# Kernel optimization log

Measured on AMD Instinct MI355X. Metric: run time of the kernel, lower is better.

The kernel has to match this reference:

```python
import jax, jax.numpy as jnp
import numpy as np

B, H, L, DK = 1, 16, 2048, 64
F_FACTOR = 64            # f
MAX_SEQ = 2048           # max_seq_len
RB = MAX_SEQ // F_FACTOR # 32, out dim of f_b


def setup_inputs() -> dict:
    key = jax.random.key(0)
    ks = jax.random.split(key, 6)
    q = jax.random.normal(ks[0], (B, H, L, DK), dtype=jnp.float32)
    v = jax.random.normal(ks[1], (B, H, L, DK), dtype=jnp.float32)
    # nn.Linear weights: [out_features, in_features]
    Wa = jax.random.normal(ks[2], (F_FACTOR, DK), dtype=jnp.float32) / np.sqrt(DK)
    ba = jax.random.normal(ks[3], (F_FACTOR,), dtype=jnp.float32) * 0.02
    Wb = jax.random.normal(ks[4], (RB, DK), dtype=jnp.float32) / np.sqrt(DK)
    bb = jax.random.normal(ks[5], (RB,), dtype=jnp.float32) * 0.02
    return {"q": q, "v": v, "Wa": Wa, "ba": ba, "Wb": Wb, "bb": bb, "len_q": L}


def reference(q, v, Wa, ba, Wb, bb, len_q):
    f = Wa.shape[0]            # f
    rb = Wb.shape[0]           # max_seq_len // f
    # h_a: repeat each of the f factor channels (max_seq_len//f) times -> [B,H,L,max_seq_len], slice to len_q
    h_a = jnp.repeat(q @ Wa.T + ba, rb, axis=-1)[..., :len_q]
    # h_b: repeat each of the (max_seq_len//f) channels f times
    h_b = jnp.repeat(q @ Wb.T + bb, f, axis=-1)[..., :len_q]
    # dense_attn = h_a @ h_b^T  -> [B,H,L,L]
    dense_attn = jnp.einsum('bhik,bhjk->bhij', h_a, h_b)
    # mask=None path; dropout inactive (eval / p=0)
    dense_attn = jax.nn.softmax(dense_attn, axis=-1)
    output = jnp.matmul(dense_attn, v)  # [B,H,L,DK]
    return (output, dense_attn)
```

## Files before the change

kernel.cpp:

```cpp
#include <hip/hip_runtime.h>
#include <hip/hip_bf16.h>


#define HN 16
#define LN 2048
#define KR 32

typedef __attribute__((ext_vector_type(8))) short bf16x8;
typedef __attribute__((ext_vector_type(4))) float f32x4;

__device__ __forceinline__ float b2f(unsigned short u) {
    return __uint_as_float(((unsigned int)u) << 16);
}
__device__ __forceinline__ unsigned short f2b(float f) {
    __hip_bfloat16 h = __float2bfloat16(f);
    return *reinterpret_cast<unsigned short*>(&h);
}

__device__ __forceinline__ void bar_lds() {
    __builtin_amdgcn_sched_barrier(0);
    asm volatile("s_waitcnt lgkmcnt(0)" ::: "memory");
    __builtin_amdgcn_s_barrier();
    __builtin_amdgcn_sched_barrier(0);
}

#define TILE_B 4096
#define TILE_V 4096

__global__ __launch_bounds__(256) void k_cb(
    const float* __restrict__ q,
    const float* __restrict__ Wa, const float* __restrict__ ba,
    const float* __restrict__ Wb, const float* __restrict__ bb,
    unsigned short* __restrict__ Chi, unsigned short* __restrict__ Clo,
    unsigned short* __restrict__ TileB)
{
    __shared__ float sWa[64 * 64];
    __shared__ float sWb[32 * 64];
    __shared__ float sba[64];
    __shared__ float sbb[32];
    const int tid = threadIdx.x;
    for (int i = tid; i < 64 * 64; i += 256) sWa[i] = Wa[i];
    for (int i = tid; i < 32 * 64; i += 256) sWb[i] = Wb[i];
    if (tid < 64) sba[tid] = ba[tid];
    if (tid < 32) sbb[tid] = bb[tid];
    __syncthreads();

    const int t = blockIdx.x * 256 + tid;
    const int row = t >> 2, kg = t & 3, mh = kg * 8;
    const int h = row >> 11, i = row & 2047;
    const int jc = i >> 6, c = i & 63;

    float qf[64];
    const float4* q4p = reinterpret_cast<const float4*>(q + (size_t)row * 64);
    #pragma unroll
    for (int k4 = 0; k4 < 16; ++k4) {
        float4 u = q4p[k4];
        qf[4*k4+0] = u.x; qf[4*k4+1] = u.y; qf[4*k4+2] = u.z; qf[4*k4+3] = u.w;
    }
    unsigned short chb[8], clb[8], bhb[8], blb[8];
    #pragma unroll
    for (int mi = 0; mi < 8; ++mi) {
        const int m = mh + mi;
        float a0 = sba[2*m], a1 = sba[2*m+1], bv = sbb[m];
        const float4* wa0 = reinterpret_cast<const float4*>(&sWa[(2*m) * 64]);
        const float4* wa1 = reinterpret_cast<const float4*>(&sWa[(2*m+1) * 64]);
        const float4* wb0 = reinterpret_cast<const float4*>(&sWb[m * 64]);
        #pragma unroll
        for (int k4 = 0; k4 < 16; ++k4) {
            float4 w0 = wa0[k4], w1 = wa1[k4], w2 = wb0[k4];
            float x0 = qf[4*k4], x1 = qf[4*k4+1], x2 = qf[4*k4+2], x3 = qf[4*k4+3];
            a0 = fmaf(x0, w0.x, a0); a0 = fmaf(x1, w0.y, a0);
            a0 = fmaf(x2, w0.z, a0); a0 = fmaf(x3, w0.w, a0);
            a1 = fmaf(x0, w1.x, a1); a1 = fmaf(x1, w1.y, a1);
            a1 = fmaf(x2, w1.z, a1); a1 = fmaf(x3, w1.w, a1);
            bv = fmaf(x0, w2.x, bv); bv = fmaf(x1, w2.y, bv);
            bv = fmaf(x2, w2.z, bv); bv = fmaf(x3, w2.w, bv);
        }
        float cc = 32.f * (a0 + a1);
        unsigned short ch = f2b(cc);
        chb[mi] = ch; clb[mi] = f2b(cc - b2f(ch));
        unsigned short bh = f2b(bv);
        bhb[mi] = bh; blb[mi] = f2b(bv - b2f(bh));
    }
    *reinterpret_cast<uint4*>(Chi + (size_t)row * KR + mh) = *reinterpret_cast<uint4*>(chb);
    *reinterpret_cast<uint4*>(Clo + (size_t)row * KR + mh) = *reinterpret_cast<uint4*>(clb);
    unsigned short* tb = TileB + (size_t)(h * 32 + jc) * TILE_B + (kg * 64 + c) * 8;
    *reinterpret_cast<uint4*>(tb)        = *reinterpret_cast<uint4*>(bhb);
    *reinterpret_cast<uint4*>(tb + 2048) = *reinterpret_cast<uint4*>(blb);
}

__global__ __launch_bounds__(256) void k_vtc(
    const float* __restrict__ v, unsigned short* __restrict__ TileV)
{
    __shared__ unsigned short sv[64 * 66];
    const int tid = threadIdx.x;
    const int h = blockIdx.x >> 5, jc = blockIdx.x & 31;
    const float* src = v + (size_t)(h * LN + jc * 64) * 64;
    for (int i = tid; i < 4096; i += 256)
        sv[(i >> 6) * 66 + (i & 63)] = f2b(src[i]);
    __syncthreads();
    unsigned short* vt = TileV + (size_t)(h * 32 + jc) * TILE_V;
    #pragma unroll
    for (int it = 0; it < 2; ++it) {
        const int gi = tid + it * 256;
        const int jg = gi >> 6, d = gi & 63;
        unsigned short g8[8];
        #pragma unroll
        for (int jj = 0; jj < 8; ++jj)
            g8[jj] = sv[(jg * 8 + jj) * 66 + d];
        *reinterpret_cast<uint4*>(vt + (jg * 64 + d) * 8) = *reinterpret_cast<uint4*>(g8);
    }
}

#define PS_STRIDE 1032
__global__ __launch_bounds__(256, 2) void k_fuse(
    const unsigned short* __restrict__ Chi, const unsigned short* __restrict__ Clo,
    const unsigned short* __restrict__ TileB, const unsigned short* __restrict__ TileV,
    float* __restrict__ outO, float* __restrict__ outP)
{
    __shared__ unsigned short ps[16 * PS_STRIDE];
    __shared__ float sRedM[4][16];
    __shared__ float sRedL[4][16];

    const int b = blockIdx.x;
    const int h = (b & 7) * 2 + (b >> 10);
    const int tile = (b >> 3) & 127;
    const int tid = threadIdx.x, w = tid >> 6, lane = tid & 63;
    const int quad = lane >> 4, n16 = lane & 15;
    const int rbase = tile * 16;
    const int hL = h * LN;

    const bf16x8 ahi = *reinterpret_cast<const bf16x8*>(Chi + (size_t)(hL + rbase + n16) * KR + quad * 8);
    const bf16x8 alo = *reinterpret_cast<const bf16x8*>(Clo + (size_t)(hL + rbase + n16) * KR + quad * 8);

    const unsigned short* bTile = TileB + (size_t)(h * 32) * TILE_B;
    const unsigned short* vTile = TileV + (size_t)(h * 32) * TILE_V;
    const int fragW = (quad * 64 + w * 16 + n16) * 8;

    f32x4 zero = {0.f, 0.f, 0.f, 0.f};
    f32x4 sS[32];

    #pragma unroll
    for (int jc = 0; jc < 32; ++jc) {
        const unsigned short* g = bTile + jc * TILE_B;
        bf16x8 bhi = *reinterpret_cast<const bf16x8*>(g + fragW);
        bf16x8 blo = *reinterpret_cast<const bf16x8*>(g + 2048 + fragW);
        f32x4 acc = zero;
        acc = __builtin_amdgcn_mfma_f32_16x16x32_bf16(ahi, bhi, acc, 0, 0, 0);
        acc = __builtin_amdgcn_mfma_f32_16x16x32_bf16(ahi, blo, acc, 0, 0, 0);
        acc = __builtin_amdgcn_mfma_f32_16x16x32_bf16(alo, bhi, acc, 0, 0, 0);
        sS[jc] = acc;
    }

    float mr[4], li[4], liS;
    const int srow = w * 4 + quad;
    {
        float m0[4];
        #pragma unroll
        for (int r = 0; r < 4; ++r) {
            float mm = sS[0][r];
            #pragma unroll
            for (int jc = 1; jc < 32; ++jc) mm = fmaxf(mm, sS[jc][r]);
            #pragma unroll
            for (int off = 1; off <= 8; off <<= 1)
                mm = fmaxf(mm, __shfl_xor(mm, off, 64));
            m0[r] = mm;
        }
        if (n16 == 0) {
            #pragma unroll
            for (int r = 0; r < 4; ++r) sRedM[w][quad * 4 + r] = m0[r];
        }
        bar_lds();
        #pragma unroll
        for (int r = 0; r < 4; ++r)
            mr[r] = fmaxf(fmaxf(sRedM[0][quad*4+r], sRedM[1][quad*4+r]),
                          fmaxf(sRedM[2][quad*4+r], sRedM[3][quad*4+r]));
        float l0[4] = {0.f, 0.f, 0.f, 0.f};
        #pragma unroll
        for (int jc = 0; jc < 32; ++jc) {
            #pragma unroll
            for (int r = 0; r < 4; ++r) {
                float p = __expf(sS[jc][r] - mr[r]);
                sS[jc][r] = p;
                l0[r] += p;
            }
        }
        #pragma unroll
        for (int r = 0; r < 4; ++r) {
            float ll = l0[r];
            #pragma unroll
            for (int off = 1; off <= 8; off <<= 1)
                ll += __shfl_xor(ll, off, 64);
            l0[r] = ll;
        }
        if (n16 == 0) {
            #pragma unroll
            for (int r = 0; r < 4; ++r) sRedL[w][quad * 4 + r] = l0[r];
        }
        bar_lds();
        #pragma unroll
        for (int r = 0; r < 4; ++r)
            li[r] = 1.f / (sRedL[0][quad*4+r] + sRedL[1][quad*4+r]
                         + sRedL[2][quad*4+r] + sRedL[3][quad*4+r]);
        liS = 1.f / (sRedL[0][srow] + sRedL[1][srow]
                   + sRedL[2][srow] + sRedL[3][srow]);
    }

    f32x4 o0 = zero, o1 = zero;
    float* prow = outP + (size_t)(hL + rbase + srow) * LN;
    #pragma unroll
    for (int half = 0; half < 2; ++half) {
        if (half) bar_lds();
        const int jc0 = half * 16;
        #pragma unroll
        for (int ji = 0; ji < 16; ++ji) {
            #pragma unroll
            for (int r = 0; r < 4; ++r)
                ps[(quad * 4 + r) * PS_STRIDE + ji * 64 + w * 16 + n16]
                    = f2b(sS[jc0 + ji][r]);
        }
        bar_lds();

        #pragma unroll
        for (int ji = 0; ji < 16; ++ji) {
            const int jc = jc0 + ji;
            const unsigned short* vt = vTile + jc * TILE_V;
            bf16x8 pa0 = *reinterpret_cast<const bf16x8*>(
                ps + n16 * PS_STRIDE + ji * 64 + quad * 8);
            bf16x8 pa1 = *reinterpret_cast<const bf16x8*>(
                ps + n16 * PS_STRIDE + ji * 64 + 32 + quad * 8);
            bf16x8 vb0 = *reinterpret_cast<const bf16x8*>(
                vt + (quad * 64 + w * 16 + n16) * 8);
            bf16x8 vb1 = *reinterpret_cast<const bf16x8*>(
                vt + ((4 + quad) * 64 + w * 16 + n16) * 8);
            o0 = __builtin_amdgcn_mfma_f32_16x16x32_bf16(pa0, vb0, o0, 0, 0, 0);
            o1 = __builtin_amdgcn_mfma_f32_16x16x32_bf16(pa1, vb1, o1, 0, 0, 0);
        }

        #pragma unroll
        for (int ch = 0; ch < 16; ++ch) {
            const unsigned short* pp = ps + srow * PS_STRIDE + ch * 64 + n16 * 4;
            uint2 u = *reinterpret_cast<const uint2*>(pp);
            f32x4 pv;
            pv[0] = __uint_as_float((u.x & 0xffffu) << 16) * liS;
            pv[1] = __uint_as_float(u.x & 0xffff0000u) * liS;
            pv[2] = __uint_as_float((u.y & 0xffffu) << 16) * liS;
            pv[3] = __uint_as_float(u.y & 0xffff0000u) * liS;
            __builtin_nontemporal_store(pv, reinterpret_cast<f32x4*>(
                prow + half * 1024 + ch * 64 + n16 * 4));
        }
    }
    #pragma unroll
    for (int r = 0; r < 4; ++r)
        __builtin_nontemporal_store((o0[r] + o1[r]) * li[r],
            &outO[(size_t)(hL + rbase + quad * 4 + r) * 64 + w * 16 + n16]);
}

extern "C" void kernel_launch(void* const* d_in, const int* in_sizes, int n_in,
                              void* d_out, int out_size, void* d_ws, size_t ws_size,
                              hipStream_t stream)
{
    (void)in_sizes; (void)n_in; (void)out_size; (void)ws_size;
    const float* q  = (const float*)d_in[0];
    const float* v  = (const float*)d_in[1];
    const float* Wa = (const float*)d_in[2];
    const float* ba = (const float*)d_in[3];
    const float* Wb = (const float*)d_in[4];
    const float* bb = (const float*)d_in[5];

    float* out = (float*)d_out;
    char* wsb = (char*)d_ws;
    const size_t MB = 1024 * 1024;
    unsigned short* Chi   = (unsigned short*)(wsb);
    unsigned short* Clo   = (unsigned short*)(wsb + 2 * MB);
    unsigned short* TileB = (unsigned short*)(wsb + 4 * MB);
    unsigned short* TileV = (unsigned short*)(wsb + 8 * MB);

    float* outO = out;
    float* outP = out + (size_t)HN * LN * 64;

    hipLaunchKernelGGL(k_cb, dim3(512), dim3(256), 0, stream,
                       q, Wa, ba, Wb, bb, Chi, Clo, TileB);
    hipLaunchKernelGGL(k_vtc, dim3(512), dim3(256), 0, stream, v, TileV);
    hipLaunchKernelGGL(k_fuse, dim3(2048), dim3(256), 0, stream,
                       Chi, Clo, TileB, TileV, outO, outP);
}
```

Before: 370.5 us.

## Merge prep kernels, pack softmax probs to bf16 registers, raise occupancy

```diff
diff --git a/kernel.cpp b/kernel.cpp
--- a/kernel.cpp
+++ b/kernel.cpp
@@ -27,18 +27,41 @@
 #define TILE_B 4096
 #define TILE_V 4096
 
-__global__ __launch_bounds__(256) void k_cb(
-    const float* __restrict__ q,
+__global__ __launch_bounds__(256) void k_prep(
+    const float* __restrict__ q, const float* __restrict__ v,
     const float* __restrict__ Wa, const float* __restrict__ ba,
     const float* __restrict__ Wb, const float* __restrict__ bb,
     unsigned short* __restrict__ Chi, unsigned short* __restrict__ Clo,
-    unsigned short* __restrict__ TileB)
+    unsigned short* __restrict__ TileB, unsigned short* __restrict__ TileV)
 {
     __shared__ float sWa[64 * 64];
     __shared__ float sWb[32 * 64];
     __shared__ float sba[64];
     __shared__ float sbb[32];
     const int tid = threadIdx.x;
+
+    if (blockIdx.x >= 512) {
+        unsigned short* sv = reinterpret_cast<unsigned short*>(sWa);
+        const int bb_ = blockIdx.x - 512;
+        const int h = bb_ >> 5, jc = bb_ & 31;
+        const float* src = v + (size_t)(h * LN + jc * 64) * 64;
+        for (int i = tid; i < 4096; i += 256)
+            sv[(i >> 6) * 66 + (i & 63)] = f2b(src[i]);
+        __syncthreads();
+        unsigned short* vt = TileV + (size_t)(h * 32 + jc) * TILE_V;
+        #pragma unroll
+        for (int it = 0; it < 2; ++it) {
+            const int gi = tid + it * 256;
+            const int jg = gi >> 6, d = gi & 63;
+            unsigned short g8[8];
+            #pragma unroll
+            for (int jj = 0; jj < 8; ++jj)
+                g8[jj] = sv[(jg * 8 + jj) * 66 + d];
+            *reinterpret_cast<uint4*>(vt + (jg * 64 + d) * 8) = *reinterpret_cast<uint4*>(g8);
+        }
+        return;
+    }
+
     for (int i = tid; i < 64 * 64; i += 256) sWa[i] = Wa[i];
     for (int i = tid; i < 32 * 64; i += 256) sWb[i] = Wb[i];
     if (tid < 64) sba[tid] = ba[tid];
@@ -89,31 +112,8 @@
     *reinterpret_cast<uint4*>(tb + 2048) = *reinterpret_cast<uint4*>(blb);
 }
 
-__global__ __launch_bounds__(256) void k_vtc(
-    const float* __restrict__ v, unsigned short* __restrict__ TileV)
-{
-    __shared__ unsigned short sv[64 * 66];
-    const int tid = threadIdx.x;
-    const int h = blockIdx.x >> 5, jc = blockIdx.x & 31;
-    const float* src = v + (size_t)(h * LN + jc * 64) * 64;
-    for (int i = tid; i < 4096; i += 256)
-        sv[(i >> 6) * 66 + (i & 63)] = f2b(src[i]);
-    __syncthreads();
-    unsigned short* vt = TileV + (size_t)(h * 32 + jc) * TILE_V;
-    #pragma unroll
-    for (int it = 0; it < 2; ++it) {
-        const int gi = tid + it * 256;
-        const int jg = gi >> 6, d = gi & 63;
-        unsigned short g8[8];
-        #pragma unroll
-        for (int jj = 0; jj < 8; ++jj)
-            g8[jj] = sv[(jg * 8 + jj) * 66 + d];
-        *reinterpret_cast<uint4*>(vt + (jg * 64 + d) * 8) = *reinterpret_cast<uint4*>(g8);
-    }
-}
-
 #define PS_STRIDE 1032
-__global__ __launch_bounds__(256, 2) void k_fuse(
+__global__ __launch_bounds__(256, 3) void k_fuse(
     const unsigned short* __restrict__ Chi, const unsigned short* __restrict__ Clo,
     const unsigned short* __restrict__ TileB, const unsigned short* __restrict__ TileV,
     float* __restrict__ outO, float* __restrict__ outP)
@@ -147,15 +147,16 @@
         bf16x8 blo = *reinterpret_cast<const bf16x8*>(g + 2048 + fragW);
         f32x4 acc = zero;
         acc = __builtin_amdgcn_mfma_f32_16x16x32_bf16(ahi, bhi, acc, 0, 0, 0);
+        acc = __builtin_amdgcn_mfma_f32_16x16x32_bf16(alo, bhi, acc, 0, 0, 0);
         acc = __builtin_amdgcn_mfma_f32_16x16x32_bf16(ahi, blo, acc, 0, 0, 0);
-        acc = __builtin_amdgcn_mfma_f32_16x16x32_bf16(alo, bhi, acc, 0, 0, 0);
         sS[jc] = acc;
     }
 
-    float mr[4], li[4], liS;
+    unsigned int pk[64];
+    float liS;
     const int srow = w * 4 + quad;
     {
-        float m0[4];
+        float m0[4], mr[4];
         #pragma unroll
         for (int r = 0; r < 4; ++r) {
             float mm = sS[0][r];
@@ -178,12 +179,13 @@
         float l0[4] = {0.f, 0.f, 0.f, 0.f};
         #pragma unroll
         for (int jc = 0; jc < 32; ++jc) {
-            #pragma unroll
-            for (int r = 0; r < 4; ++r) {
-                float p = __expf(sS[jc][r] - mr[r]);
-                sS[jc][r] = p;
-                l0[r] += p;
-            }
+            float p0 = __expf(sS[jc][0] - mr[0]);
+            float p1 = __expf(sS[jc][1] - mr[1]);
+            float p2 = __expf(sS[jc][2] - mr[2]);
+            float p3 = __expf(sS[jc][3] - mr[3]);
+            l0[0] += p0; l0[1] += p1; l0[2] += p2; l0[3] += p3;
+            pk[jc*2]   = ((unsigned int)f2b(p1) << 16) | (unsigned int)f2b(p0);
+            pk[jc*2+1] = ((unsigned int)f2b(p3) << 16) | (unsigned int)f2b(p2);
         }
         #pragma unroll
         for (int r = 0; r < 4; ++r) {
@@ -198,10 +200,6 @@
             for (int r = 0; r < 4; ++r) sRedL[w][quad * 4 + r] = l0[r];
         }
         bar_lds();
-        #pragma unroll
-        for (int r = 0; r < 4; ++r)
-            li[r] = 1.f / (sRedL[0][quad*4+r] + sRedL[1][quad*4+r]
-                         + sRedL[2][quad*4+r] + sRedL[3][quad*4+r]);
         liS = 1.f / (sRedL[0][srow] + sRedL[1][srow]
                    + sRedL[2][srow] + sRedL[3][srow]);
     }
@@ -214,12 +212,29 @@
         const int jc0 = half * 16;
         #pragma unroll
         for (int ji = 0; ji < 16; ++ji) {
-            #pragma unroll
-            for (int r = 0; r < 4; ++r)
-                ps[(quad * 4 + r) * PS_STRIDE + ji * 64 + w * 16 + n16]
-                    = f2b(sS[jc0 + ji][r]);
+            const int jc = jc0 + ji;
+            #pragma unroll
+            for (int r = 0; r < 4; ++r) {
+                const unsigned int pkv = pk[jc*2 + (r>>1)];
+                const unsigned short pv16 = (r & 1) ? (unsigned short)(pkv >> 16)
+                                                    : (unsigned short)(pkv & 0xffffu);
+                ps[(quad * 4 + r) * PS_STRIDE + ji * 64 + w * 16 + n16] = pv16;
+            }
         }
         bar_lds();
+
+        #pragma unroll
+        for (int ch = 0; ch < 16; ++ch) {
+            const unsigned short* pp = ps + srow * PS_STRIDE + ch * 64 + n16 * 4;
+            uint2 u = *reinterpret_cast<const uint2*>(pp);
+            f32x4 pv;
+            pv[0] = __uint_as_float((u.x & 0xffffu) << 16) * liS;
+            pv[1] = __uint_as_float(u.x & 0xffff0000u) * liS;
+            pv[2] = __uint_as_float((u.y & 0xffffu) << 16) * liS;
+            pv[3] = __uint_as_float(u.y & 0xffff0000u) * liS;
+            __builtin_nontemporal_store(pv, reinterpret_cast<f32x4*>(
+                prow + half * 1024 + ch * 64 + n16 * 4));
+        }
 
         #pragma unroll
         for (int ji = 0; ji < 16; ++ji) {
@@ -236,24 +251,14 @@
             o0 = __builtin_amdgcn_mfma_f32_16x16x32_bf16(pa0, vb0, o0, 0, 0, 0);
             o1 = __builtin_amdgcn_mfma_f32_16x16x32_bf16(pa1, vb1, o1, 0, 0, 0);
         }
-
-        #pragma unroll
-        for (int ch = 0; ch < 16; ++ch) {
-            const unsigned short* pp = ps + srow * PS_STRIDE + ch * 64 + n16 * 4;
-            uint2 u = *reinterpret_cast<const uint2*>(pp);
-            f32x4 pv;
-            pv[0] = __uint_as_float((u.x & 0xffffu) << 16) * liS;
-            pv[1] = __uint_as_float(u.x & 0xffff0000u) * liS;
-            pv[2] = __uint_as_float((u.y & 0xffffu) << 16) * liS;
-            pv[3] = __uint_as_float(u.y & 0xffff0000u) * liS;
-            __builtin_nontemporal_store(pv, reinterpret_cast<f32x4*>(
-                prow + half * 1024 + ch * 64 + n16 * 4));
-        }
-    }
-    #pragma unroll
-    for (int r = 0; r < 4; ++r)
-        __builtin_nontemporal_store((o0[r] + o1[r]) * li[r],
+    }
+    #pragma unroll
+    for (int r = 0; r < 4; ++r) {
+        const float li = 1.f / (sRedL[0][quad*4+r] + sRedL[1][quad*4+r]
+                              + sRedL[2][quad*4+r] + sRedL[3][quad*4+r]);
+        __builtin_nontemporal_store((o0[r] + o1[r]) * li,
             &outO[(size_t)(hL + rbase + quad * 4 + r) * 64 + w * 16 + n16]);
+    }
 }
 
 extern "C" void kernel_launch(void* const* d_in, const int* in_sizes, int n_in,
@@ -279,9 +284,8 @@
     float* outO = out;
     float* outP = out + (size_t)HN * LN * 64;
 
-    hipLaunchKernelGGL(k_cb, dim3(512), dim3(256), 0, stream,
-                       q, Wa, ba, Wb, bb, Chi, Clo, TileB);
-    hipLaunchKernelGGL(k_vtc, dim3(512), dim3(256), 0, stream, v, TileV);
+    hipLaunchKernelGGL(k_prep, dim3(1024), dim3(256), 0, stream,
+                       q, v, Wa, ba, Wb, bb, Chi, Clo, TileB, TileV);
     hipLaunchKernelGGL(k_fuse, dim3(2048), dim3(256), 0, stream,
                        Chi, Clo, TileB, TileV, outO, outP);
 }
```

Result: no change. 376.2 us (+1.5%).

## Split fused softmax-attention block into 8 waves across key halves

Applied to the files above, without the earlier changes.

```diff
diff --git a/kernel.cpp b/kernel.cpp
--- a/kernel.cpp
+++ b/kernel.cpp
@@ -112,21 +112,24 @@
     }
 }
 
-#define PS_STRIDE 1032
-__global__ __launch_bounds__(256, 2) void k_fuse(
+#define PS_STRIDE 2056
+__global__ __launch_bounds__(512, 4) void k_fuse(
     const unsigned short* __restrict__ Chi, const unsigned short* __restrict__ Clo,
     const unsigned short* __restrict__ TileB, const unsigned short* __restrict__ TileV,
     float* __restrict__ outO, float* __restrict__ outP)
 {
     __shared__ unsigned short ps[16 * PS_STRIDE];
-    __shared__ float sRedM[4][16];
-    __shared__ float sRedL[4][16];
+    __shared__ float sRedM[8][16];
+    __shared__ float sRedL[8][16];
+    __shared__ float sO[4 * 16 * 16];
 
     const int b = blockIdx.x;
     const int h = (b & 7) * 2 + (b >> 10);
     const int tile = (b >> 3) & 127;
     const int tid = threadIdx.x, w = tid >> 6, lane = tid & 63;
     const int quad = lane >> 4, n16 = lane & 15;
+    const int jh = w >> 2, sub = w & 3;
+    const int dg = w & 3;
     const int rbase = tile * 16;
     const int hL = h * LN;
 
@@ -135,32 +138,32 @@
 
     const unsigned short* bTile = TileB + (size_t)(h * 32) * TILE_B;
     const unsigned short* vTile = TileV + (size_t)(h * 32) * TILE_V;
-    const int fragW = (quad * 64 + w * 16 + n16) * 8;
+    const int fragW = (quad * 64 + sub * 16 + n16) * 8;
 
     f32x4 zero = {0.f, 0.f, 0.f, 0.f};
-    f32x4 sS[32];
-
-    #pragma unroll
-    for (int jc = 0; jc < 32; ++jc) {
-        const unsigned short* g = bTile + jc * TILE_B;
+    f32x4 sS[16];
+
+    #pragma unroll
+    for (int ji = 0; ji < 16; ++ji) {
+        const unsigned short* g = bTile + (jh * 16 + ji) * TILE_B;
         bf16x8 bhi = *reinterpret_cast<const bf16x8*>(g + fragW);
         bf16x8 blo = *reinterpret_cast<const bf16x8*>(g + 2048 + fragW);
         f32x4 acc = zero;
         acc = __builtin_amdgcn_mfma_f32_16x16x32_bf16(ahi, bhi, acc, 0, 0, 0);
+        acc = __builtin_amdgcn_mfma_f32_16x16x32_bf16(alo, bhi, acc, 0, 0, 0);
         acc = __builtin_amdgcn_mfma_f32_16x16x32_bf16(ahi, blo, acc, 0, 0, 0);
-        acc = __builtin_amdgcn_mfma_f32_16x16x32_bf16(alo, bhi, acc, 0, 0, 0);
-        sS[jc] = acc;
-    }
-
-    float mr[4], li[4], liS;
-    const int srow = w * 4 + quad;
+        sS[ji] = acc;
+    }
+
+    float li[4], liS;
+    const int srow = w * 2 + (lane >> 5);
     {
-        float m0[4];
+        float m0[4], mr[4];
         #pragma unroll
         for (int r = 0; r < 4; ++r) {
             float mm = sS[0][r];
             #pragma unroll
-            for (int jc = 1; jc < 32; ++jc) mm = fmaxf(mm, sS[jc][r]);
+            for (int ji = 1; ji < 16; ++ji) mm = fmaxf(mm, sS[ji][r]);
             #pragma unroll
             for (int off = 1; off <= 8; off <<= 1)
                 mm = fmaxf(mm, __shfl_xor(mm, off, 64));
@@ -172,16 +175,20 @@
         }
         bar_lds();
         #pragma unroll
-        for (int r = 0; r < 4; ++r)
-            mr[r] = fmaxf(fmaxf(sRedM[0][quad*4+r], sRedM[1][quad*4+r]),
-                          fmaxf(sRedM[2][quad*4+r], sRedM[3][quad*4+r]));
+        for (int r = 0; r < 4; ++r) {
+            float a = fmaxf(fmaxf(sRedM[0][quad*4+r], sRedM[1][quad*4+r]),
+                            fmaxf(sRedM[2][quad*4+r], sRedM[3][quad*4+r]));
+            float c = fmaxf(fmaxf(sRedM[4][quad*4+r], sRedM[5][quad*4+r]),
+                            fmaxf(sRedM[6][quad*4+r], sRedM[7][quad*4+r]));
+            mr[r] = fmaxf(a, c);
+        }
         float l0[4] = {0.f, 0.f, 0.f, 0.f};
         #pragma unroll
-        for (int jc = 0; jc < 32; ++jc) {
+        for (int ji = 0; ji < 16; ++ji) {
             #pragma unroll
             for (int r = 0; r < 4; ++r) {
-                float p = __expf(sS[jc][r] - mr[r]);
-                sS[jc][r] = p;
+                float p = __expf(sS[ji][r] - mr[r]);
+                sS[ji][r] = p;
                 l0[r] += p;
             }
         }
@@ -201,59 +208,71 @@
         #pragma unroll
         for (int r = 0; r < 4; ++r)
             li[r] = 1.f / (sRedL[0][quad*4+r] + sRedL[1][quad*4+r]
-                         + sRedL[2][quad*4+r] + sRedL[3][quad*4+r]);
-        liS = 1.f / (sRedL[0][srow] + sRedL[1][srow]
-                   + sRedL[2][srow] + sRedL[3][srow]);
-    }
-
-    f32x4 o0 = zero, o1 = zero;
-    float* prow = outP + (size_t)(hL + rbase + srow) * LN;
-    #pragma unroll
-    for (int half = 0; half < 2; ++half) {
-        if (half) bar_lds();
-        const int jc0 = half * 16;
-        #pragma unroll
-        for (int ji = 0; ji < 16; ++ji) {
-            #pragma unroll
-            for (int r = 0; r < 4; ++r)
-                ps[(quad * 4 + r) * PS_STRIDE + ji * 64 + w * 16 + n16]
-                    = f2b(sS[jc0 + ji][r]);
-        }
-        bar_lds();
-
-        #pragma unroll
-        for (int ji = 0; ji < 16; ++ji) {
-            const int jc = jc0 + ji;
-            const unsigned short* vt = vTile + jc * TILE_V;
-            bf16x8 pa0 = *reinterpret_cast<const bf16x8*>(
-                ps + n16 * PS_STRIDE + ji * 64 + quad * 8);
-            bf16x8 pa1 = *reinterpret_cast<const bf16x8*>(
-                ps + n16 * PS_STRIDE + ji * 64 + 32 + quad * 8);
-            bf16x8 vb0 = *reinterpret_cast<const bf16x8*>(
-                vt + (quad * 64 + w * 16 + n16) * 8);
-            bf16x8 vb1 = *reinterpret_cast<const bf16x8*>(
-                vt + ((4 + quad) * 64 + w * 16 + n16) * 8);
-            o0 = __builtin_amdgcn_mfma_f32_16x16x32_bf16(pa0, vb0, o0, 0, 0, 0);
-            o1 = __builtin_amdgcn_mfma_f32_16x16x32_bf16(pa1, vb1, o1, 0, 0, 0);
-        }
-
+                         + sRedL[2][quad*4+r] + sRedL[3][quad*4+r]
+                         + sRedL[4][quad*4+r] + sRedL[5][quad*4+r]
+                         + sRedL[6][quad*4+r] + sRedL[7][quad*4+r]);
+        liS = 1.f / (sRedL[0][srow] + sRedL[1][srow] + sRedL[2][srow]
+                   + sRedL[3][srow] + sRedL[4][srow] + sRedL[5][srow]
+                   + sRedL[6][srow] + sRedL[7][srow]);
+    }
+
+    #pragma unroll
+    for (int ji = 0; ji < 16; ++ji) {
+        const int col = (jh * 16 + ji) * 64 + sub * 16 + n16;
+        #pragma unroll
+        for (int r = 0; r < 4; ++r)
+            ps[(quad * 4 + r) * PS_STRIDE + col] = f2b(sS[ji][r]);
+    }
+    bar_lds();
+
+    {
+        const int c5 = lane & 31;
+        float* prow = outP + (size_t)(hL + rbase + srow) * LN;
+        const unsigned short* psr = ps + srow * PS_STRIDE;
         #pragma unroll
         for (int ch = 0; ch < 16; ++ch) {
-            const unsigned short* pp = ps + srow * PS_STRIDE + ch * 64 + n16 * 4;
-            uint2 u = *reinterpret_cast<const uint2*>(pp);
+            uint2 u = *reinterpret_cast<const uint2*>(psr + ch * 128 + c5 * 4);
             f32x4 pv;
             pv[0] = __uint_as_float((u.x & 0xffffu) << 16) * liS;
             pv[1] = __uint_as_float(u.x & 0xffff0000u) * liS;
             pv[2] = __uint_as_float((u.y & 0xffffu) << 16) * liS;
             pv[3] = __uint_as_float(u.y & 0xffff0000u) * liS;
             __builtin_nontemporal_store(pv, reinterpret_cast<f32x4*>(
-                prow + half * 1024 + ch * 64 + n16 * 4));
-        }
-    }
-    #pragma unroll
-    for (int r = 0; r < 4; ++r)
-        __builtin_nontemporal_store((o0[r] + o1[r]) * li[r],
-            &outO[(size_t)(hL + rbase + quad * 4 + r) * 64 + w * 16 + n16]);
+                prow + ch * 128 + c5 * 4));
+        }
+    }
+
+    f32x4 o0 = zero, o1 = zero;
+    #pragma unroll
+    for (int ji = 0; ji < 16; ++ji) {
+        const int jc = jh * 16 + ji;
+        const unsigned short* vt = vTile + jc * TILE_V;
+        bf16x8 pa0 = *reinterpret_cast<const bf16x8*>(
+            ps + n16 * PS_STRIDE + jc * 64 + quad * 8);
+        bf16x8 pa1 = *reinterpret_cast<const bf16x8*>(
+            ps + n16 * PS_STRIDE + jc * 64 + 32 + quad * 8);
+        bf16x8 vb0 = *reinterpret_cast<const bf16x8*>(
+            vt + (quad * 64 + dg * 16 + n16) * 8);
+        bf16x8 vb1 = *reinterpret_cast<const bf16x8*>(
+            vt + ((4 + quad) * 64 + dg * 16 + n16) * 8);
+        o0 = __builtin_amdgcn_mfma_f32_16x16x32_bf16(pa0, vb0, o0, 0, 0, 0);
+        o1 = __builtin_amdgcn_mfma_f32_16x16x32_bf16(pa1, vb1, o1, 0, 0, 0);
+    }
+
+    if (jh == 1) {
+        #pragma unroll
+        for (int r = 0; r < 4; ++r)
+            sO[dg * 256 + (quad * 4 + r) * 16 + n16] = o0[r] + o1[r];
+    }
+    bar_lds();
+    if (jh == 0) {
+        #pragma unroll
+        for (int r = 0; r < 4; ++r) {
+            float ov = o0[r] + o1[r] + sO[dg * 256 + (quad * 4 + r) * 16 + n16];
+            __builtin_nontemporal_store(ov * li[r],
+                &outO[(size_t)(hL + rbase + quad * 4 + r) * 64 + dg * 16 + n16]);
+        }
+    }
 }
 
 extern "C" void kernel_launch(void* const* d_in, const int* in_sizes, int n_in,
@@ -282,6 +301,6 @@
     hipLaunchKernelGGL(k_cb, dim3(512), dim3(256), 0, stream,
                        q, Wa, ba, Wb, bb, Chi, Clo, TileB);
     hipLaunchKernelGGL(k_vtc, dim3(512), dim3(256), 0, stream, v, TileV);
-    hipLaunchKernelGGL(k_fuse, dim3(2048), dim3(256), 0, stream,
+    hipLaunchKernelGGL(k_fuse, dim3(2048), dim3(512), 0, stream,
                        Chi, Clo, TileB, TileV, outO, outP);
 }
```

After: 387.8 us. 1.05x slower.
